# Performance work log

Measured on AMD Instinct MI355X. Metric: run time of the kernel, lower is better.

Reference implementation:

```python
import jax, jax.numpy as jnp
import numpy as np

N_NODES = 50000
N_RAND_EDGES = 800000
K_HEADS = 4
D = 64
EPS = 1e-8


def setup_inputs() -> dict:
    key = jax.random.key(0)
    k1, k2, k3, k4, k5, k6 = jax.random.split(key, 6)
    x = jax.random.normal(k1, (N_NODES, D), dtype=jnp.float32)
    # edge_index without self loops (module removes then re-adds them), then append self loops
    dst = jax.random.randint(k2, (N_RAND_EDGES,), 0, N_NODES)
    off = jax.random.randint(k3, (N_RAND_EDGES,), 1, N_NODES)
    src = (dst + off) % N_NODES  # guaranteed src != dst
    loops = jnp.arange(N_NODES)
    adj = jnp.stack([jnp.concatenate([dst, loops]), jnp.concatenate([src, loops])]).astype(jnp.int64)
    e = jax.random.uniform(k4, (N_NODES, K_HEADS), dtype=jnp.float32)
    stdv = 1.0 / np.sqrt(D)
    weights = jax.random.uniform(k5, (K_HEADS, D, D), minval=-stdv, maxval=stdv, dtype=jnp.float32)
    # xavier_uniform(gain=1.414) on [K, 2D, 1]
    bound = 1.414 * np.sqrt(6.0 / (2 * D + 1))
    a = jax.random.uniform(k6, (K_HEADS, 2 * D, 1), minval=-bound, maxval=bound, dtype=jnp.float32)
    return {"x": x, "adj": adj, "e": e, "weights": weights, "a": a}


def reference(x, adj, e, weights, a):
    N = x.shape[0]
    O = weights.shape[2]
    dst, src = adj[0], adj[1]  # aggregation destination = adj[0], source = adj[1]
    # per-head projection: h[k] = x @ weights[k]  -> [K, N, O]
    h = jnp.einsum('nd,kdo->kno', x, weights)
    # split attention vector: edge_h @ a == <h[dst], a[:O]> + <h[src], a[O:]>
    a_dst = a[:, :O, 0]   # [K, O]
    a_src = a[:, O:, 0]   # [K, O]
    alpha_dst = jnp.einsum('kno,ko->kn', h, a_dst)  # [K, N]
    alpha_src = jnp.einsum('kno,ko->kn', h, a_src)  # [K, N]
    logits = jax.nn.leaky_relu(alpha_dst[:, dst] + alpha_src[:, src], 0.01)  # [K, E]
    # global (per-head) max subtraction, as in the original
    edge_e = jnp.exp(logits - jnp.max(logits, axis=1, keepdims=True))  # [K, E]
    seg = lambda v: jax.ops.segment_sum(v, dst, num_segments=N)
    denom = jax.vmap(seg)(edge_e) + EPS                                 # [K, N]
    num = jax.vmap(seg)(edge_e[:, :, None] * h[:, src])                 # [K, N, O]
    outputs = num / denom[:, :, None]                                   # [K, N, O]
    out = jnp.einsum('nk,kno->no', e, outputs)                          # mixture over K
    return out + x  # residual
```

## Files before the change

### kernel.cpp

```cpp
#include <hip/hip_runtime.h>
#include <hip/hip_bf16.h>

#define KH 4
#define DIM 64
#define EPSV 1e-8f
#define BIN_BLKS 768

typedef __attribute__((ext_vector_type(8))) short bf16x8;
typedef __attribute__((ext_vector_type(4))) float f32x4;

__device__ __forceinline__ float lrelu(float s) { return s > 0.0f ? s : 0.01f * s; }
__device__ __forceinline__ float blo(unsigned u) { return __uint_as_float(u << 16); }
__device__ __forceinline__ float bhi(unsigned u) { return __uint_as_float(u & 0xFFFF0000u); }
__device__ __forceinline__ unsigned short f2b(float f) {
    unsigned u = __float_as_uint(f);
    u += 0x7FFFu + ((u >> 16) & 1u);
    return (unsigned short)(u >> 16);
}

__global__ void __launch_bounds__(256, 4)
k_hidden(const float* __restrict__ x,
         const float* __restrict__ W,
         const float* __restrict__ a,
         __hip_bfloat16* __restrict__ h,
         float* __restrict__ adst,
         float* __restrict__ asrc,
         int* __restrict__ cnt, int N) {
    int t = threadIdx.x;
    int gid = blockIdx.x * 256 + t;
    if (gid < N) cnt[gid] = 0;
    int k = t >> 6;
    int l = t & 63;
    int s = l & 15;
    int q = l >> 4;
    int n0 = blockIdx.x * 16;

    const float* Wk = W + k * DIM * DIM;
    bf16x8 Bf[4][2];
#pragma unroll
    for (int tile = 0; tile < 4; ++tile)
#pragma unroll
        for (int c = 0; c < 2; ++c) {
            const float* wp = Wk + (size_t)(32 * c + 8 * q) * DIM + 16 * tile + s;
#pragma unroll
            for (int j = 0; j < 8; ++j)
                Bf[tile][c][j] = (short)f2b(wp[(size_t)j * DIM]);
        }
    float ad[4], as_[4];
#pragma unroll
    for (int tile = 0; tile < 4; ++tile) {
        ad[tile]  = a[k * 2 * DIM + 16 * tile + s];
        as_[tile] = a[k * 2 * DIM + DIM + 16 * tile + s];
    }

    bf16x8 Af[2];
#pragma unroll
    for (int c = 0; c < 2; ++c) {
        const float* xp = x + (size_t)(n0 + s) * DIM + 32 * c + 8 * q;
#pragma unroll
        for (int j = 0; j < 8; ++j) Af[c][j] = (short)f2b(xp[j]);
    }

    f32x4 acc[4];
#pragma unroll
    for (int tile = 0; tile < 4; ++tile) {
        acc[tile] = (f32x4){0.f, 0.f, 0.f, 0.f};
#pragma unroll
        for (int c = 0; c < 2; ++c)
            acc[tile] = __builtin_amdgcn_mfma_f32_16x16x32_bf16(
                Af[c], Bf[tile][c], acc[tile], 0, 0, 0);
    }

#pragma unroll
    for (int r = 0; r < 4; ++r) {
        float vd = 0.f, vs = 0.f;
#pragma unroll
        for (int tile = 0; tile < 4; ++tile) {
            vd = fmaf(acc[tile][r], ad[tile], vd);
            vs = fmaf(acc[tile][r], as_[tile], vs);
        }
#pragma unroll
        for (int off = 1; off < 16; off <<= 1) {
            vd += __shfl_xor(vd, off);
            vs += __shfl_xor(vs, off);
        }
        if (s == 0) {
            int n = n0 + 4 * q + r;
            adst[n * KH + k] = vd;
            asrc[n * KH + k] = vs;
        }
    }

    __shared__ unsigned short hb[16 * DIM * KH];
#pragma unroll
    for (int tile = 0; tile < 4; ++tile)
#pragma unroll
        for (int r = 0; r < 4; ++r) {
            int n = 4 * q + r, o = 16 * tile + s;
            hb[(n * DIM + o) * KH + k] = f2b(acc[tile][r]);
        }
    __syncthreads();
    const uint2* hb2 = (const uint2*)hb;
    uint2* h2 = (uint2*)h;
#pragma unroll
    for (int it = 0; it < 4; ++it) {
        int i = it * 256 + t;
        h2[(size_t)n0 * DIM + i] = hb2[i];
    }
}

__global__ void k_bin(const int* __restrict__ dst, const int* __restrict__ src,
                      const float4* __restrict__ adst4, const float4* __restrict__ asrc4,
                      int* __restrict__ cnt,
                      int* __restrict__ bsrc, uint2* __restrict__ bw,
                      int cap, int E) {
    int T = gridDim.x * blockDim.x;
    int tid = blockIdx.x * blockDim.x + threadIdx.x;
    int e = tid;
    for (; e + 3 * T < E; e += 4 * T) {
        int e0 = e, e1 = e + T, e2 = e + 2 * T, e3 = e + 3 * T;
        int dn0 = dst[e0], dn1 = dst[e1], dn2 = dst[e2], dn3 = dst[e3];
        int sn0 = src[e0], sn1 = src[e1], sn2 = src[e2], sn3 = src[e3];
        int sl0 = atomicAdd(&cnt[dn0], 1);
        int sl1 = atomicAdd(&cnt[dn1], 1);
        int sl2 = atomicAdd(&cnt[dn2], 1);
        int sl3 = atomicAdd(&cnt[dn3], 1);
        float4 ad0 = adst4[dn0], as0 = asrc4[sn0];
        float4 ad1 = adst4[dn1], as1 = asrc4[sn1];
        float4 ad2 = adst4[dn2], as2 = asrc4[sn2];
        float4 ad3 = adst4[dn3], as3 = asrc4[sn3];
#define EMIT(sl, dn, sn, ad, as)                                              \
        if (sl < cap) {                                                       \
            uint2 wp;                                                         \
            wp.x = (unsigned)f2b(__expf(lrelu(ad.x + as.x))) |                \
                   ((unsigned)f2b(__expf(lrelu(ad.y + as.y))) << 16);         \
            wp.y = (unsigned)f2b(__expf(lrelu(ad.z + as.z))) |                \
                   ((unsigned)f2b(__expf(lrelu(ad.w + as.w))) << 16);         \
            size_t base = (size_t)dn * cap + sl;                              \
            bsrc[base] = sn;                                                  \
            bw[base] = wp;                                                    \
        }
        EMIT(sl0, dn0, sn0, ad0, as0)
        EMIT(sl1, dn1, sn1, ad1, as1)
        EMIT(sl2, dn2, sn2, ad2, as2)
        EMIT(sl3, dn3, sn3, ad3, as3)
    }
    for (; e < E; e += T) {
        int dn = dst[e], sn = src[e];
        int sl = atomicAdd(&cnt[dn], 1);
        float4 ad = adst4[dn], as = asrc4[sn];
        EMIT(sl, dn, sn, ad, as)
    }
#undef EMIT
}

__global__ void k_aggr(const int* __restrict__ cnt, const int* __restrict__ bsrc,
                       const uint2* __restrict__ bw,
                       const __hip_bfloat16* __restrict__ h,
                       const float* __restrict__ efeat, const float* __restrict__ x,
                       float* __restrict__ out, int cap, int N) {
    int n = blockIdx.x * 4 + (threadIdx.x >> 6);
    if (n >= N) return;
    int o = threadIdx.x & 63;
    int deg = cnt[n]; if (deg > cap) deg = cap;
    const int* bs = bsrc + (size_t)n * cap;
    const uint2* bwp = bw + (size_t)n * cap;
    const uint2* h2 = (const uint2*)h;
    float v0 = 0.f, v1 = 0.f, v2 = 0.f, v3 = 0.f;
    float d0 = 0.f, d1 = 0.f, d2 = 0.f, d3 = 0.f;
#define ACC(p, hv)                                                            \
    {                                                                         \
        float w;                                                              \
        w = blo(p.x); v0 = fmaf(w, blo(hv.x), v0); d0 += w;                   \
        w = bhi(p.x); v1 = fmaf(w, bhi(hv.x), v1); d1 += w;                   \
        w = blo(p.y); v2 = fmaf(w, blo(hv.y), v2); d2 += w;                   \
        w = bhi(p.y); v3 = fmaf(w, bhi(hv.y), v3); d3 += w;                   \
    }
    int i = 0;
    for (; i + 4 <= deg; i += 4) {
        int s0 = bs[i + 0], s1 = bs[i + 1], s2 = bs[i + 2], s3 = bs[i + 3];
        uint2 p0 = bwp[i + 0], p1 = bwp[i + 1], p2 = bwp[i + 2], p3 = bwp[i + 3];
        uint2 a0 = h2[(size_t)s0 * DIM + o];
        uint2 a1 = h2[(size_t)s1 * DIM + o];
        uint2 a2 = h2[(size_t)s2 * DIM + o];
        uint2 a3 = h2[(size_t)s3 * DIM + o];
        ACC(p0, a0) ACC(p1, a1) ACC(p2, a2) ACC(p3, a3)
    }
    for (; i < deg; ++i) {
        int sn = bs[i];
        uint2 p = bwp[i];
        uint2 hv = h2[(size_t)sn * DIM + o];
        ACC(p, hv)
    }
#undef ACC
    float4 ef = ((const float4*)efeat)[n];
    float c0 = ef.x / (d0 + EPSV), c1 = ef.y / (d1 + EPSV);
    float c2 = ef.z / (d2 + EPSV), c3 = ef.w / (d3 + EPSV);
    size_t oi = (size_t)n * DIM + o;
    out[oi] = x[oi] + c0 * v0 + c1 * v1 + c2 * v2 + c3 * v3;
}

extern "C" void kernel_launch(void* const* d_in, const int* in_sizes, int n_in,
                              void* d_out, int out_size, void* d_ws, size_t ws_size,
                              hipStream_t stream) {
    const float* x = (const float*)d_in[0];
    const int* adj = (const int*)d_in[1];
    const float* efeat = (const float*)d_in[2];
    const float* W = (const float*)d_in[3];
    const float* a = (const float*)d_in[4];
    float* out = (float*)d_out;

    int N = in_sizes[0] / DIM;
    int E = in_sizes[1] / 2;
    const int* dst = adj;
    const int* src = adj + E;
    int nbhid = (N + 15) / 16;

    __hip_bfloat16* h = (__hip_bfloat16*)d_ws;
    float* adst = (float*)(h + (size_t)N * DIM * KH);
    float* asrc = adst + (size_t)N * KH;
    int* cnt = (int*)(asrc + (size_t)N * KH);
    int* bsrc = cnt + N;
    size_t used = (size_t)((char*)bsrc - (char*)d_ws);
    int cap = (int)((ws_size - used) / ((size_t)N * 12));
    if (cap > 64) cap = 64;
    uint2* bw = (uint2*)(bsrc + (size_t)N * cap);

    k_hidden<<<nbhid, 256, 0, stream>>>(x, W, a, h, adst, asrc, cnt, N);

    k_bin<<<BIN_BLKS, 256, 0, stream>>>(dst, src, (const float4*)adst,
                                        (const float4*)asrc, cnt,
                                        bsrc, bw, cap, E);

    k_aggr<<<(N + 3) / 4, 256, 0, stream>>>(cnt, bsrc, bw, h, efeat, x, out, cap, N);
}
```

Before: 207.6 us.

## Store hidden features as FP8 e4m3 and pack edge slots into one uint4

The per-head hidden features are now quantized to FP8 e4m3 instead of bf16, so each gather in the aggregation kernel reads 4 bytes per lane instead of 8. The separate source-index and weight arrays are merged into a single 16-byte slot per edge, padded with an unused word. The intent is to cut the random-gather bandwidth in the aggregation, which dominates the cost. In exchange the FP8 rounding costs accuracy, and each slot grows from 12 to 16 bytes, which shrinks the available per-node capacity.

```diff
diff --git a/kernel.cpp b/kernel.cpp
--- a/kernel.cpp
+++ b/kernel.cpp
@@ -8,6 +8,7 @@
 
 typedef __attribute__((ext_vector_type(8))) short bf16x8;
 typedef __attribute__((ext_vector_type(4))) float f32x4;
+typedef __attribute__((ext_vector_type(2))) float f32x2;
 
 __device__ __forceinline__ float lrelu(float s) { return s > 0.0f ? s : 0.01f * s; }
 __device__ __forceinline__ float blo(unsigned u) { return __uint_as_float(u << 16); }
@@ -18,11 +19,49 @@
     return (unsigned short)(u >> 16);
 }
 
+__device__ __forceinline__ unsigned char f2e4m3(float f) {
+    unsigned u = __float_as_uint(f);
+    unsigned sgn = (u >> 31) << 7;
+    float af = fabsf(f);
+    if (af >= 0.015625f) {
+        unsigned mag = u & 0x7FFFFFFFu;
+        unsigned biased = mag - (120u << 23);
+        unsigned em = biased >> 20;
+        unsigned rem = biased & 0xFFFFFu;
+        em += (rem > 0x80000u) ? 1u : ((rem == 0x80000u) ? (em & 1u) : 0u);
+        if (em > 126u) em = 126u;
+        return (unsigned char)(sgn | em);
+    } else {
+        int m = (int)rintf(af * 512.0f);
+        if (m >= 8) return (unsigned char)(sgn | 8u);
+        return (unsigned char)(sgn | (unsigned)m);
+    }
+}
+
+__device__ __forceinline__ void e4m3x4_to_f32(unsigned v, float& h0, float& h1,
+                                              float& h2, float& h3) {
+#if __has_builtin(__builtin_amdgcn_cvt_pk_f32_fp8)
+    f32x2 lo = __builtin_amdgcn_cvt_pk_f32_fp8(v, false);
+    f32x2 hi = __builtin_amdgcn_cvt_pk_f32_fp8(v, true);
+    h0 = lo.x; h1 = lo.y; h2 = hi.x; h3 = hi.y;
+#else
+    auto dec = [](unsigned b) -> float {
+        unsigned s = b >> 7, em = b & 0x7Fu;
+        float r;
+        if (em >= 8u) r = __uint_as_float((em << 20) + (120u << 23));
+        else r = (float)em * 0.001953125f;
+        return s ? -r : r;
+    };
+    h0 = dec(v & 0xFF); h1 = dec((v >> 8) & 0xFF);
+    h2 = dec((v >> 16) & 0xFF); h3 = dec(v >> 24);
+#endif
+}
+
 __global__ void __launch_bounds__(256, 4)
 k_hidden(const float* __restrict__ x,
          const float* __restrict__ W,
          const float* __restrict__ a,
-         __hip_bfloat16* __restrict__ h,
+         unsigned* __restrict__ h8,
          float* __restrict__ adst,
          float* __restrict__ asrc,
          int* __restrict__ cnt, int N) {
@@ -91,28 +130,26 @@
         }
     }
 
-    __shared__ unsigned short hb[16 * DIM * KH];
+    __shared__ unsigned char hb[16 * DIM * KH];
 #pragma unroll
     for (int tile = 0; tile < 4; ++tile)
 #pragma unroll
         for (int r = 0; r < 4; ++r) {
             int n = 4 * q + r, o = 16 * tile + s;
-            hb[(n * DIM + o) * KH + k] = f2b(acc[tile][r]);
+            hb[(n * DIM + o) * KH + k] = f2e4m3(acc[tile][r]);
         }
     __syncthreads();
-    const uint2* hb2 = (const uint2*)hb;
-    uint2* h2 = (uint2*)h;
+    const unsigned* hb4 = (const unsigned*)hb;
 #pragma unroll
     for (int it = 0; it < 4; ++it) {
         int i = it * 256 + t;
-        h2[(size_t)n0 * DIM + i] = hb2[i];
+        h8[(size_t)n0 * DIM + i] = hb4[i];
     }
 }
 
 __global__ void k_bin(const int* __restrict__ dst, const int* __restrict__ src,
                       const float4* __restrict__ adst4, const float4* __restrict__ asrc4,
-                      int* __restrict__ cnt,
-                      int* __restrict__ bsrc, uint2* __restrict__ bw,
+                      int* __restrict__ cnt, uint4* __restrict__ slots,
                       int cap, int E) {
     int T = gridDim.x * blockDim.x;
     int tid = blockIdx.x * blockDim.x + threadIdx.x;
@@ -131,14 +168,14 @@
         float4 ad3 = adst4[dn3], as3 = asrc4[sn3];
 #define EMIT(sl, dn, sn, ad, as)                                              \
         if (sl < cap) {                                                       \
-            uint2 wp;                                                         \
-            wp.x = (unsigned)f2b(__expf(lrelu(ad.x + as.x))) |                \
+            uint4 sv;                                                         \
+            sv.x = (unsigned)sn;                                              \
+            sv.y = (unsigned)f2b(__expf(lrelu(ad.x + as.x))) |                \
                    ((unsigned)f2b(__expf(lrelu(ad.y + as.y))) << 16);         \
-            wp.y = (unsigned)f2b(__expf(lrelu(ad.z + as.z))) |                \
+            sv.z = (unsigned)f2b(__expf(lrelu(ad.z + as.z))) |                \
                    ((unsigned)f2b(__expf(lrelu(ad.w + as.w))) << 16);         \
-            size_t base = (size_t)dn * cap + sl;                              \
-            bsrc[base] = sn;                                                  \
-            bw[base] = wp;                                                    \
+            sv.w = 0u;                                                        \
+            slots[(size_t)dn * cap + sl] = sv;                                \
         }
         EMIT(sl0, dn0, sn0, ad0, as0)
         EMIT(sl1, dn1, sn1, ad1, as1)
@@ -154,43 +191,40 @@
 #undef EMIT
 }
 
-__global__ void k_aggr(const int* __restrict__ cnt, const int* __restrict__ bsrc,
-                       const uint2* __restrict__ bw,
-                       const __hip_bfloat16* __restrict__ h,
+__global__ void k_aggr(const int* __restrict__ cnt, const uint4* __restrict__ slots,
+                       const unsigned* __restrict__ h8,
                        const float* __restrict__ efeat, const float* __restrict__ x,
                        float* __restrict__ out, int cap, int N) {
     int n = blockIdx.x * 4 + (threadIdx.x >> 6);
     if (n >= N) return;
     int o = threadIdx.x & 63;
     int deg = cnt[n]; if (deg > cap) deg = cap;
-    const int* bs = bsrc + (size_t)n * cap;
-    const uint2* bwp = bw + (size_t)n * cap;
-    const uint2* h2 = (const uint2*)h;
+    const uint4* bs = slots + (size_t)n * cap;
     float v0 = 0.f, v1 = 0.f, v2 = 0.f, v3 = 0.f;
     float d0 = 0.f, d1 = 0.f, d2 = 0.f, d3 = 0.f;
-#define ACC(p, hv)                                                            \
+#define ACC(sv, hv)                                                           \
     {                                                                         \
+        float h0, h1, h2, h3;                                                 \
+        e4m3x4_to_f32(hv, h0, h1, h2, h3);                                    \
         float w;                                                              \
-        w = blo(p.x); v0 = fmaf(w, blo(hv.x), v0); d0 += w;                   \
-        w = bhi(p.x); v1 = fmaf(w, bhi(hv.x), v1); d1 += w;                   \
-        w = blo(p.y); v2 = fmaf(w, blo(hv.y), v2); d2 += w;                   \
-        w = bhi(p.y); v3 = fmaf(w, bhi(hv.y), v3); d3 += w;                   \
+        w = blo(sv.y); v0 = fmaf(w, h0, v0); d0 += w;                         \
+        w = bhi(sv.y); v1 = fmaf(w, h1, v1); d1 += w;                         \
+        w = blo(sv.z); v2 = fmaf(w, h2, v2); d2 += w;                         \
+        w = bhi(sv.z); v3 = fmaf(w, h3, v3); d3 += w;                         \
     }
     int i = 0;
     for (; i + 4 <= deg; i += 4) {
-        int s0 = bs[i + 0], s1 = bs[i + 1], s2 = bs[i + 2], s3 = bs[i + 3];
-        uint2 p0 = bwp[i + 0], p1 = bwp[i + 1], p2 = bwp[i + 2], p3 = bwp[i + 3];
-        uint2 a0 = h2[(size_t)s0 * DIM + o];
-        uint2 a1 = h2[(size_t)s1 * DIM + o];
-        uint2 a2 = h2[(size_t)s2 * DIM + o];
-        uint2 a3 = h2[(size_t)s3 * DIM + o];
-        ACC(p0, a0) ACC(p1, a1) ACC(p2, a2) ACC(p3, a3)
+        uint4 s0 = bs[i + 0], s1 = bs[i + 1], s2 = bs[i + 2], s3 = bs[i + 3];
+        unsigned a0 = h8[(size_t)s0.x * DIM + o];
+        unsigned a1 = h8[(size_t)s1.x * DIM + o];
+        unsigned a2 = h8[(size_t)s2.x * DIM + o];
+        unsigned a3 = h8[(size_t)s3.x * DIM + o];
+        ACC(s0, a0) ACC(s1, a1) ACC(s2, a2) ACC(s3, a3)
     }
     for (; i < deg; ++i) {
-        int sn = bs[i];
-        uint2 p = bwp[i];
-        uint2 hv = h2[(size_t)sn * DIM + o];
-        ACC(p, hv)
+        uint4 sv = bs[i];
+        unsigned hv = h8[(size_t)sv.x * DIM + o];
+        ACC(sv, hv)
     }
 #undef ACC
     float4 ef = ((const float4*)efeat)[n];
@@ -216,21 +250,19 @@
     const int* src = adj + E;
     int nbhid = (N + 15) / 16;
 
-    __hip_bfloat16* h = (__hip_bfloat16*)d_ws;
-    float* adst = (float*)(h + (size_t)N * DIM * KH);
+    unsigned* h8 = (unsigned*)d_ws;
+    float* adst = (float*)(h8 + (size_t)N * DIM);
     float* asrc = adst + (size_t)N * KH;
     int* cnt = (int*)(asrc + (size_t)N * KH);
-    int* bsrc = cnt + N;
-    size_t used = (size_t)((char*)bsrc - (char*)d_ws);
-    int cap = (int)((ws_size - used) / ((size_t)N * 12));
+    uint4* slots = (uint4*)(cnt + N);
+    size_t used = (size_t)((char*)slots - (char*)d_ws);
+    int cap = (int)((ws_size - used) / ((size_t)N * 16));
     if (cap > 64) cap = 64;
-    uint2* bw = (uint2*)(bsrc + (size_t)N * cap);
-
-    k_hidden<<<nbhid, 256, 0, stream>>>(x, W, a, h, adst, asrc, cnt, N);
+
+    k_hidden<<<nbhid, 256, 0, stream>>>(x, W, a, h8, adst, asrc, cnt, N);
 
     k_bin<<<BIN_BLKS, 256, 0, stream>>>(dst, src, (const float4*)adst,
-                                        (const float4*)asrc, cnt,
-                                        bsrc, bw, cap, E);
-
-    k_aggr<<<(N + 3) / 4, 256, 0, stream>>>(cnt, bsrc, bw, h, efeat, x, out, cap, N);
-}
+                                        (const float4*)asrc, cnt, slots, cap, E);
+
+    k_aggr<<<(N + 3) / 4, 256, 0, stream>>>(cnt, slots, h8, efeat, x, out, cap, N);
+}
```

Result: faster. 184.3 us (-11.2%).
